# Optimization experiments

Measured on AMD Instinct MI355X. Metric: run time of the kernel, lower is better.

The kernel has to match this reference:

```python
import jax, jax.numpy as jnp
import numpy as np


def setup_inputs() -> dict:
    key = jax.random.key(0)
    k1, k2, k3, k4 = jax.random.split(key, 4)
    B, T, C, H = 8, 2048, 1024, 1024
    return {
        "x": jax.random.normal(k1, (B, T, C), dtype=jnp.float32),
        "Wk": jax.random.normal(k2, (H, C), dtype=jnp.float32),
        "Wq": jax.random.normal(k3, (H, C), dtype=jnp.float32),
        "Wv": jax.random.normal(k4, (H, C), dtype=jnp.float32),
    }


def reference(x, Wk, Wq, Wv):
    # x: [B, T, C]; Wk/Wq/Wv: [H, C] (torch Linear stores [fan_out, fan_in])
    B, T, C = x.shape
    k = jnp.einsum('btc,hc->bth', x, Wk)  # [B, T, H]
    q = jnp.einsum('btc,hc->bth', x, Wq)
    v = jnp.einsum('btc,hc->bth', x, Wv)
    # NOTE: source scales by n_embd (C) ** -0.5, not head_size
    wei = jnp.einsum('bth,bsh->bts', q, k) * (C ** -0.5)  # [B, T, T]
    causal = jnp.tril(jnp.ones((T, T), dtype=bool))
    wei = jnp.where(causal, wei, -jnp.inf)
    wei = jax.nn.softmax(wei, axis=-1)
    # Dropout omitted (inference behavior; p=0.5 train-only in source)
    out = jnp.einsum('bts,bsh->bth', wei, v)  # [B, T, H]
    return (out, wei)
```

## Files before the change

### kernel.cpp

```cpp
#include <hip/hip_runtime.h>
#include <hip/hip_bf16.h>


#define BB 8
#define TT 2048
#define CC 1024
#define HH 1024
#define BT (BB * TT)

typedef _Float16 f16x8 __attribute__((ext_vector_type(8)));
typedef _Float16 f16x4 __attribute__((ext_vector_type(4)));
typedef float f32x4 __attribute__((ext_vector_type(4)));

#define AS1 __attribute__((address_space(1)))
#define AS3 __attribute__((address_space(3)))

__device__ __forceinline__ void gld16(const _Float16* g, _Float16* lds) {
    __builtin_amdgcn_global_load_lds((AS1 const unsigned int*)g,
                                     (AS3 unsigned int*)lds, 16, 0, 0);
}

__global__ __launch_bounds__(256) void split_kernel(
    const float* __restrict__ src, _Float16* __restrict__ dh,
    _Float16* __restrict__ dl, int n)
{
    int i = (blockIdx.x * 256 + threadIdx.x) * 4;
    if (i >= n) return;
    float4 v = *(const float4*)(src + i);
    f16x4 h, l;
    h[0] = (_Float16)v.x; l[0] = (_Float16)(v.x - (float)h[0]);
    h[1] = (_Float16)v.y; l[1] = (_Float16)(v.y - (float)h[1]);
    h[2] = (_Float16)v.z; l[2] = (_Float16)(v.z - (float)h[2]);
    h[3] = (_Float16)v.w; l[3] = (_Float16)(v.w - (float)h[3]);
    *(f16x4*)&dh[i] = h;
    *(f16x4*)&dl[i] = l;
}

__global__ __launch_bounds__(256) void splitT_kernel(
    const float* __restrict__ W, _Float16* __restrict__ th,
    _Float16* __restrict__ tl)
{
    __shared__ float L[64][65];
    const int h0 = blockIdx.x * 64;
    const int c0 = blockIdx.y * 64;
    const int tid = threadIdx.x;
    {
        const int hl = tid >> 2;
        const int cs = (tid & 3) * 16;
#pragma unroll
        for (int jj = 0; jj < 16; jj += 4) {
            float4 v = *(const float4*)&W[(size_t)(h0 + hl) * CC + c0 + cs + jj];
            L[cs + jj + 0][hl] = v.x;
            L[cs + jj + 1][hl] = v.y;
            L[cs + jj + 2][hl] = v.z;
            L[cs + jj + 3][hl] = v.w;
        }
    }
    __syncthreads();
    const int c  = tid >> 2;
    const int hs = (tid & 3) * 16;
    f16x8 hv0, hv1, lv0, lv1;
#pragma unroll
    for (int i = 0; i < 8; ++i) {
        float a = L[c][hs + i], b = L[c][hs + 8 + i];
        hv0[i] = (_Float16)a; lv0[i] = (_Float16)(a - (float)hv0[i]);
        hv1[i] = (_Float16)b; lv1[i] = (_Float16)(b - (float)hv1[i]);
    }
    size_t o = (size_t)(c0 + c) * HH + h0 + hs;
    *(f16x8*)&th[o] = hv0; *(f16x8*)&th[o + 8] = hv1;
    *(f16x8*)&tl[o] = lv0; *(f16x8*)&tl[o + 8] = lv1;
}

__global__ __launch_bounds__(256, 2) void mm_kernel(
    const _Float16* __restrict__ aH, const _Float16* __restrict__ aL,
    const _Float16* __restrict__ bH, const _Float16* __restrict__ bL,
    _Float16* __restrict__ mtH, _Float16* __restrict__ mtL)
{
    __shared__ _Float16 Ah[4096], Al[4096], Bh[4096], Bl[4096];

    const int n0 = blockIdx.x * 128;
    const int m0 = blockIdx.y * 128;

    const int tid  = threadIdx.x;
    const int r0   = tid & 127;
    const int k0   = tid >> 7;
    const int wave = tid >> 6;
    const int lane = tid & 63;
    const int quad = lane >> 4;
    const int lrow = lane & 15;
    const int wr   = (wave >> 1) * 64;
    const int wc   = (wave & 1) * 64;

    const size_t ga = (size_t)(m0 + r0) * HH + k0 * 8;
    const size_t gb = (size_t)(n0 + r0) * HH + k0 * 8;
    const int lds0 = tid * 8, lds1 = (tid + 256) * 8;

    f32x4 acc[4][4] = {};

    for (int kc = 0; kc < HH; kc += 32) {
        __syncthreads();
        gld16(aH + ga + kc,      &Ah[lds0]);
        gld16(aH + ga + kc + 16, &Ah[lds1]);
        gld16(aL + ga + kc,      &Al[lds0]);
        gld16(aL + ga + kc + 16, &Al[lds1]);
        gld16(bH + gb + kc,      &Bh[lds0]);
        gld16(bH + gb + kc + 16, &Bh[lds1]);
        gld16(bL + gb + kc,      &Bl[lds0]);
        gld16(bL + gb + kc + 16, &Bl[lds1]);
        __syncthreads();

        f16x8 ahf[4], alf[4], bhf[4], blf[4];
#pragma unroll
        for (int i = 0; i < 4; ++i) {
            ahf[i] = *(const f16x8*)&Ah[(quad * 128 + wr + i * 16 + lrow) * 8];
            alf[i] = *(const f16x8*)&Al[(quad * 128 + wr + i * 16 + lrow) * 8];
            bhf[i] = *(const f16x8*)&Bh[(quad * 128 + wc + i * 16 + lrow) * 8];
            blf[i] = *(const f16x8*)&Bl[(quad * 128 + wc + i * 16 + lrow) * 8];
        }
#pragma unroll
        for (int i = 0; i < 4; ++i)
#pragma unroll
            for (int j = 0; j < 4; ++j) {
                acc[i][j] = __builtin_amdgcn_mfma_f32_16x16x32_f16(ahf[i], bhf[j], acc[i][j], 0, 0, 0);
                acc[i][j] = __builtin_amdgcn_mfma_f32_16x16x32_f16(ahf[i], blf[j], acc[i][j], 0, 0, 0);
                acc[i][j] = __builtin_amdgcn_mfma_f32_16x16x32_f16(alf[i], bhf[j], acc[i][j], 0, 0, 0);
            }
    }

#pragma unroll
    for (int i = 0; i < 4; ++i)
#pragma unroll
        for (int j = 0; j < 4; ++j) {
            int mm = m0 + wr + i * 16 + quad * 4;
            int nn = n0 + wc + j * 16 + lrow;
            f16x4 ph, pl;
#pragma unroll
            for (int r = 0; r < 4; ++r) {
                float val = acc[i][j][r];
                _Float16 h = (_Float16)val;
                ph[r] = h;
                pl[r] = (_Float16)(val - (float)h);
            }
            *(f16x4*)&mtH[(size_t)nn * CC + mm] = ph;
            *(f16x4*)&mtL[(size_t)nn * CC + mm] = pl;
        }
}

#define EPI_STRIDE 136
__global__ __launch_bounds__(256, 2) void pv_kernel(
    const _Float16* __restrict__ xh, const _Float16* __restrict__ xl,
    const _Float16* __restrict__ mtH, const _Float16* __restrict__ mtL,
    const _Float16* __restrict__ Wvh,
    _Float16* __restrict__ Ph, _Float16* __restrict__ Pl,
    _Float16* __restrict__ vT)
{
    __shared__ _Float16 S[49152];

    const int idx   = blockIdx.x;
    const int z     = idx >> 10;
    const int r     = idx & 1023;
    const int xcd   = r & 7;
    const int j7    = r >> 3;
    const int mtile = xcd * 16 + (j7 >> 3);
    const int ntile = j7 & 7;
    const int m0 = mtile * 128;
    const int n0 = ntile * 128;

    const int tid  = threadIdx.x;
    const int r0   = tid & 127;
    const int k0   = tid >> 7;
    const int wave = tid >> 6;
    const int lane = tid & 63;
    const int quad = lane >> 4;
    const int lrow = lane & 15;
    const int wr   = (wave >> 1) * 64;
    const int wc   = (wave & 1) * 64;

    const size_t ga = (size_t)(m0 + r0) * CC + k0 * 8;
    const size_t gb = (size_t)(n0 + r0) * CC + k0 * 8;
    const int lds0 = tid * 8, lds1 = (tid + 256) * 8;

    f32x4 acc[4][4] = {};

    if (z == 0) {
#define PV_STAGE0(kc_, sp_) do { \
        _Float16* Sb = S + (sp_) * 16384; \
        gld16(xh  + ga + (kc_),      &Sb[lds0]); \
        gld16(xh  + ga + (kc_) + 16, &Sb[lds1]); \
        gld16(xl  + ga + (kc_),      &Sb[4096 + lds0]); \
        gld16(xl  + ga + (kc_) + 16, &Sb[4096 + lds1]); \
        gld16(mtH + gb + (kc_),      &Sb[8192 + lds0]); \
        gld16(mtH + gb + (kc_) + 16, &Sb[8192 + lds1]); \
        gld16(mtL + gb + (kc_),      &Sb[12288 + lds0]); \
        gld16(mtL + gb + (kc_) + 16, &Sb[12288 + lds1]); \
    } while (0)
        PV_STAGE0(0, 0);
        PV_STAGE0(32, 1);
        int sl = 0;
        for (int kc = 0; kc < CC; kc += 32) {
            asm volatile("s_waitcnt vmcnt(8)" ::: "memory");
            __builtin_amdgcn_s_barrier();
            __builtin_amdgcn_sched_barrier(0);

            int kpre = kc + 64;
            if (kpre > CC - 32) kpre = CC - 32;
            int s2 = sl + 2; if (s2 >= 3) s2 -= 3;
            PV_STAGE0(kpre, s2);

            const _Float16* Ah = S + sl * 16384;
            const _Float16* Al = Ah + 4096;
            const _Float16* Bh = Ah + 8192;
            const _Float16* Bl = Ah + 12288;

            f16x8 ahf[4], alf[4], bhf[4], blf[4];
#pragma unroll
            for (int i = 0; i < 4; ++i) {
                ahf[i] = *(const f16x8*)&Ah[(quad * 128 + wr + i * 16 + lrow) * 8];
                alf[i] = *(const f16x8*)&Al[(quad * 128 + wr + i * 16 + lrow) * 8];
                bhf[i] = *(const f16x8*)&Bh[(quad * 128 + wc + i * 16 + lrow) * 8];
                blf[i] = *(const f16x8*)&Bl[(quad * 128 + wc + i * 16 + lrow) * 8];
            }
            __builtin_amdgcn_s_setprio(1);
#pragma unroll
            for (int i = 0; i < 4; ++i)
#pragma unroll
                for (int j = 0; j < 4; ++j) {
                    acc[i][j] = __builtin_amdgcn_mfma_f32_16x16x32_f16(ahf[i], bhf[j], acc[i][j], 0, 0, 0);
                    acc[i][j] = __builtin_amdgcn_mfma_f32_16x16x32_f16(ahf[i], blf[j], acc[i][j], 0, 0, 0);
                    acc[i][j] = __builtin_amdgcn_mfma_f32_16x16x32_f16(alf[i], bhf[j], acc[i][j], 0, 0, 0);
                }
            __builtin_amdgcn_s_setprio(0);

            ++sl; if (sl == 3) sl = 0;
        }
    } else {
#define PV_STAGE1(kc_, sp_) do { \
        _Float16* Sb = S + (sp_) * 8192; \
        gld16(xh  + ga + (kc_),      &Sb[lds0]); \
        gld16(xh  + ga + (kc_) + 16, &Sb[lds1]); \
        gld16(Wvh + gb + (kc_),      &Sb[4096 + lds0]); \
        gld16(Wvh + gb + (kc_) + 16, &Sb[4096 + lds1]); \
    } while (0)
        PV_STAGE1(0, 0);
        PV_STAGE1(32, 1);
        int sl = 0;
        for (int kc = 0; kc < CC; kc += 32) {
            asm volatile("s_waitcnt vmcnt(4)" ::: "memory");
            __builtin_amdgcn_s_barrier();
            __builtin_amdgcn_sched_barrier(0);

            int kpre = kc + 64;
            if (kpre > CC - 32) kpre = CC - 32;
            int s2 = sl + 2; if (s2 >= 3) s2 -= 3;
            PV_STAGE1(kpre, s2);

            const _Float16* Ah = S + sl * 8192;
            const _Float16* Bh = Ah + 4096;

            f16x8 ahf[4], bhf[4];
#pragma unroll
            for (int i = 0; i < 4; ++i) {
                ahf[i] = *(const f16x8*)&Ah[(quad * 128 + wr + i * 16 + lrow) * 8];
                bhf[i] = *(const f16x8*)&Bh[(quad * 128 + wc + i * 16 + lrow) * 8];
            }
            __builtin_amdgcn_s_setprio(1);
#pragma unroll
            for (int i = 0; i < 4; ++i)
#pragma unroll
                for (int j = 0; j < 4; ++j)
                    acc[i][j] = __builtin_amdgcn_mfma_f32_16x16x32_f16(ahf[i], bhf[j], acc[i][j], 0, 0, 0);
            __builtin_amdgcn_s_setprio(0);

            ++sl; if (sl == 3) sl = 0;
        }
    }

    asm volatile("s_waitcnt vmcnt(0)" ::: "memory");
    __syncthreads();

    if (z == 1) {
#pragma unroll
        for (int i = 0; i < 4; ++i)
#pragma unroll
            for (int j = 0; j < 4; ++j) {
                int hl = wc + j * 16 + lrow;
                int tl = wr + i * 16 + quad * 4;
                f16x4 p;
#pragma unroll
                for (int rr = 0; rr < 4; ++rr) p[rr] = (_Float16)acc[i][j][rr];
                *(f16x4*)&S[hl * EPI_STRIDE + tl] = p;
            }
        __syncthreads();
        const int bi  = mtile >> 4;
        const int t0g = (mtile & 15) * 128;
        _Float16* vb = vT + (size_t)bi * HH * TT;
#pragma unroll
        for (int rr = 0; rr < 128; rr += 16) {
            int h = rr + (tid >> 4);
            int t = (tid & 15) * 8;
            f16x8 val = *(const f16x8*)&S[h * EPI_STRIDE + t];
            *(f16x8*)&vb[(size_t)(n0 + h) * TT + t0g + t] = val;
        }
    } else {
#pragma unroll
        for (int i = 0; i < 4; ++i)
#pragma unroll
            for (int j = 0; j < 4; ++j) {
                int tl = wr + i * 16 + quad * 4;
                int cl = wc + j * 16 + lrow;
#pragma unroll
                for (int rr = 0; rr < 4; ++rr)
                    S[(tl + rr) * EPI_STRIDE + cl] = (_Float16)acc[i][j][rr];
            }
        __syncthreads();
#pragma unroll
        for (int rr = 0; rr < 128; rr += 16) {
            int t = rr + (tid >> 4);
            int c = (tid & 15) * 8;
            f16x8 val = *(const f16x8*)&S[t * EPI_STRIDE + c];
            *(f16x8*)&Ph[(size_t)(m0 + t) * CC + n0 + c] = val;
        }
        __syncthreads();
#pragma unroll
        for (int i = 0; i < 4; ++i)
#pragma unroll
            for (int j = 0; j < 4; ++j) {
                int tl = wr + i * 16 + quad * 4;
                int cl = wc + j * 16 + lrow;
#pragma unroll
                for (int rr = 0; rr < 4; ++rr) {
                    float val = acc[i][j][rr];
                    _Float16 h = (_Float16)val;
                    S[(tl + rr) * EPI_STRIDE + cl] = (_Float16)(val - (float)h);
                }
            }
        __syncthreads();
#pragma unroll
        for (int rr = 0; rr < 128; rr += 16) {
            int t = rr + (tid >> 4);
            int c = (tid & 15) * 8;
            f16x8 val = *(const f16x8*)&S[t * EPI_STRIDE + c];
            *(f16x8*)&Pl[(size_t)(m0 + t) * CC + n0 + c] = val;
        }
    }
}

__global__ __launch_bounds__(256, 2) void logits_kernel(
    const _Float16* __restrict__ Ph, const _Float16* __restrict__ Pl,
    const _Float16* __restrict__ xh, const _Float16* __restrict__ xl,
    float* __restrict__ wei)
{
    __shared__ _Float16 S[49152];

    const int id  = blockIdx.x;
    const int b   = id & 7;
    const int tri = id >> 3;
    int tt = (int)((sqrtf(8.0f * (float)tri + 1.0f) - 1.0f) * 0.5f);
    while ((tt + 1) * (tt + 2) / 2 <= tri) ++tt;
    while (tt * (tt + 1) / 2 > tri) --tt;
    const int st = tri - tt * (tt + 1) / 2;

    const size_t base = (size_t)b * TT * CC;
    float* wb = wei + (size_t)b * TT * TT;
    const int m0 = tt * 128;
    const int n0 = st * 128;

    const int tid  = threadIdx.x;
    const int r0   = tid & 127;
    const int k0   = tid >> 7;
    const int wave = tid >> 6;
    const int lane = tid & 63;
    const int quad = lane >> 4;
    const int lrow = lane & 15;
    const int wr   = (wave >> 1) * 64;
    const int wc   = (wave & 1) * 64;

    const size_t ga = base + (size_t)(m0 + r0) * CC + k0 * 8;
    const size_t gb = base + (size_t)(n0 + r0) * CC + k0 * 8;
    const int lds0 = tid * 8, lds1 = (tid + 256) * 8;

    f32x4 acc[4][4] = {};

#define LG_STAGE(kc_, sp_) do { \
    _Float16* Sb = S + (sp_) * 16384; \
    gld16(Ph + ga + (kc_),      &Sb[lds0]); \
    gld16(Ph + ga + (kc_) + 16, &Sb[lds1]); \
    gld16(Pl + ga + (kc_),      &Sb[4096 + lds0]); \
    gld16(Pl + ga + (kc_) + 16, &Sb[4096 + lds1]); \
    gld16(xh + gb + (kc_),      &Sb[8192 + lds0]); \
    gld16(xh + gb + (kc_) + 16, &Sb[8192 + lds1]); \
    gld16(xl + gb + (kc_),      &Sb[12288 + lds0]); \
    gld16(xl + gb + (kc_) + 16, &Sb[12288 + lds1]); \
} while (0)

    LG_STAGE(0, 0);
    LG_STAGE(32, 1);

    int sl = 0;
    for (int kc = 0; kc < CC; kc += 32) {
        asm volatile("s_waitcnt vmcnt(8)" ::: "memory");
        __builtin_amdgcn_s_barrier();
        __builtin_amdgcn_sched_barrier(0);

        int kpre = kc + 64;
        if (kpre > CC - 32) kpre = CC - 32;
        int s2 = sl + 2; if (s2 >= 3) s2 -= 3;
        LG_STAGE(kpre, s2);

        const _Float16* Ah = S + sl * 16384;
        const _Float16* Al = Ah + 4096;
        const _Float16* Bh = Ah + 8192;
        const _Float16* Bl = Ah + 12288;

        f16x8 ahf[4], alf[4], bhf[4], blf[4];
#pragma unroll
        for (int i = 0; i < 4; ++i) {
            ahf[i] = *(const f16x8*)&Ah[(quad * 128 + wr + i * 16 + lrow) * 8];
            alf[i] = *(const f16x8*)&Al[(quad * 128 + wr + i * 16 + lrow) * 8];
            bhf[i] = *(const f16x8*)&Bh[(quad * 128 + wc + i * 16 + lrow) * 8];
            blf[i] = *(const f16x8*)&Bl[(quad * 128 + wc + i * 16 + lrow) * 8];
        }
        __builtin_amdgcn_s_setprio(1);
#pragma unroll
        for (int i = 0; i < 4; ++i)
#pragma unroll
            for (int j = 0; j < 4; ++j) {
                acc[i][j] = __builtin_amdgcn_mfma_f32_16x16x32_f16(ahf[i], bhf[j], acc[i][j], 0, 0, 0);
                acc[i][j] = __builtin_amdgcn_mfma_f32_16x16x32_f16(ahf[i], blf[j], acc[i][j], 0, 0, 0);
                acc[i][j] = __builtin_amdgcn_mfma_f32_16x16x32_f16(alf[i], bhf[j], acc[i][j], 0, 0, 0);
            }
        __builtin_amdgcn_s_setprio(0);

        ++sl; if (sl == 3) sl = 0;
    }

    asm volatile("s_waitcnt vmcnt(0)" ::: "memory");

    const float scale = 0.03125f;
#pragma unroll
    for (int i = 0; i < 4; ++i)
#pragma unroll
        for (int j = 0; j < 4; ++j)
#pragma unroll
            for (int r = 0; r < 4; ++r) {
                int rr = wr + i * 16 + quad * 4 + r;
                int cc = wc + j * 16 + lrow;
                wb[(size_t)(m0 + rr) * TT + n0 + cc] = acc[i][j][r] * scale;
            }
}

__global__ __launch_bounds__(256) void softmax_kernel(
    float* __restrict__ wei, _Float16* __restrict__ wei16)
{
    const int t = blockIdx.x;
    const int b = blockIdx.y;
    float* row = wei + (size_t)b * TT * TT + (size_t)t * TT;
    _Float16* row16 = wei16 + (size_t)b * TT * TT + (size_t)t * TT;
    const int n = t + 1;
    const int tid = threadIdx.x;
    const int base = tid * 8;

    float vals[8];
    if (base < n) {
        float4 v0 = *(const float4*)&row[base];
        float4 v1 = *(const float4*)&row[base + 4];
        vals[0] = v0.x; vals[1] = v0.y; vals[2] = v0.z; vals[3] = v0.w;
        vals[4] = v1.x; vals[5] = v1.y; vals[6] = v1.z; vals[7] = v1.w;
    } else {
#pragma unroll
        for (int i = 0; i < 8; ++i) vals[i] = -INFINITY;
    }

    float mx = -INFINITY;
#pragma unroll
    for (int i = 0; i < 8; ++i) {
        if (base + i >= n) vals[i] = -INFINITY;
        mx = fmaxf(mx, vals[i]);
    }
#pragma unroll
    for (int off = 32; off > 0; off >>= 1)
        mx = fmaxf(mx, __shfl_down(mx, off));

    __shared__ float redm[4];
    __shared__ float reds[4];
    if ((tid & 63) == 0) redm[tid >> 6] = mx;
    __syncthreads();
    const float m = fmaxf(fmaxf(redm[0], redm[1]), fmaxf(redm[2], redm[3]));

    float sum = 0.f;
#pragma unroll
    for (int i = 0; i < 8; ++i) {
        vals[i] = __expf(vals[i] - m);
        sum += vals[i];
    }
#pragma unroll
    for (int off = 32; off > 0; off >>= 1)
        sum += __shfl_down(sum, off);
    if ((tid & 63) == 0) reds[tid >> 6] = sum;
    __syncthreads();
    const float inv = 1.0f / (reds[0] + reds[1] + reds[2] + reds[3]);

    f16x8 h;
#pragma unroll
    for (int i = 0; i < 8; ++i) {
        float w = vals[i] * inv;
        vals[i] = w;
        h[i] = (_Float16)w;
    }
    *(float4*)&row[base]     = make_float4(vals[0], vals[1], vals[2], vals[3]);
    *(float4*)&row[base + 4] = make_float4(vals[4], vals[5], vals[6], vals[7]);
    *(f16x8*)&row16[base]    = h;
}

__global__ __launch_bounds__(256, 3) void out_kernel(
    const _Float16* __restrict__ wei16, const _Float16* __restrict__ vT,
    float* __restrict__ out)
{
    __shared__ _Float16 S[24576];

    const int id = blockIdx.x;
    const int b  = id & 7;
    const int r  = id >> 3;
    const int tt = 15 - (r >> 3);
    const int nb = r & 7;

    const _Float16* wb = wei16 + (size_t)b * TT * TT;
    const _Float16* vb = vT    + (size_t)b * HH * TT;
    float*          ob = out   + (size_t)b * TT * HH;

    const int m0 = tt * 128;
    const int n0 = nb * 128;
    const int kend = (tt + 1) * 128;

    const int tid  = threadIdx.x;
    const int r0   = tid & 127;
    const int k0   = tid >> 7;
    const int wave = tid >> 6;
    const int lane = tid & 63;
    const int quad = lane >> 4;
    const int lrow = lane & 15;
    const int wr   = (wave >> 1) * 64;
    const int wc   = (wave & 1) * 64;

    const size_t ga = (size_t)(m0 + r0) * TT + k0 * 8;
    const size_t gb = (size_t)(n0 + r0) * TT + k0 * 8;
    const int lds0 = tid * 8, lds1 = (tid + 256) * 8;

    f32x4 acc[4][4] = {};

#define OUT_STAGE(kc_, sp_) do { \
    _Float16* Sb = S + (sp_) * 8192; \
    gld16(wb + ga + (kc_),      &Sb[lds0]); \
    gld16(wb + ga + (kc_) + 16, &Sb[lds1]); \
    gld16(vb + gb + (kc_),      &Sb[4096 + lds0]); \
    gld16(vb + gb + (kc_) + 16, &Sb[4096 + lds1]); \
} while (0)

    OUT_STAGE(0, 0);
    OUT_STAGE(32, 1);

    int sl = 0;
    for (int kc = 0; kc < kend; kc += 32) {
        asm volatile("s_waitcnt vmcnt(4)" ::: "memory");
        __builtin_amdgcn_s_barrier();
        __builtin_amdgcn_sched_barrier(0);

        int kpre = kc + 64;
        if (kpre > kend - 32) kpre = kend - 32;
        int s2 = sl + 2; if (s2 >= 3) s2 -= 3;
        OUT_STAGE(kpre, s2);

        const _Float16* Ah = S + sl * 8192;
        const _Float16* Bh = Ah + 4096;

        f16x8 ahf[4], bhf[4];
#pragma unroll
        for (int i = 0; i < 4; ++i) {
            ahf[i] = *(const f16x8*)&Ah[(quad * 128 + wr + i * 16 + lrow) * 8];
            bhf[i] = *(const f16x8*)&Bh[(quad * 128 + wc + i * 16 + lrow) * 8];
        }
        __builtin_amdgcn_s_setprio(1);
#pragma unroll
        for (int i = 0; i < 4; ++i)
#pragma unroll
            for (int j = 0; j < 4; ++j)
                acc[i][j] = __builtin_amdgcn_mfma_f32_16x16x32_f16(ahf[i], bhf[j], acc[i][j], 0, 0, 0);
        __builtin_amdgcn_s_setprio(0);

        ++sl; if (sl == 3) sl = 0;
    }

    asm volatile("s_waitcnt vmcnt(0)" ::: "memory");

#pragma unroll
    for (int i = 0; i < 4; ++i)
#pragma unroll
        for (int j = 0; j < 4; ++j)
#pragma unroll
            for (int r2 = 0; r2 < 4; ++r2) {
                int rr = wr + i * 16 + quad * 4 + r2;
                int cc = wc + j * 16 + lrow;
                ob[(size_t)(m0 + rr) * HH + n0 + cc] = acc[i][j][r2];
            }
}

extern "C" void kernel_launch(void* const* d_in, const int* in_sizes, int n_in,
                              void* d_out, int out_size, void* d_ws, size_t ws_size,
                              hipStream_t stream)
{
    const float* x  = (const float*)d_in[0];
    const float* Wk = (const float*)d_in[1];
    const float* Wq = (const float*)d_in[2];
    const float* Wv = (const float*)d_in[3];

    const size_t NX = (size_t)BT * CC;
    const size_t NW = (size_t)HH * CC;

    float* out = (float*)d_out;
    float* wei = out + (size_t)BT * HH;

    _Float16* WqTh = (_Float16*)out;
    _Float16* WqTl = WqTh + NW;
    _Float16* WkTh = WqTl + NW;
    _Float16* WkTl = WkTh + NW;
    _Float16* Wvh  = WkTl + NW;
    _Float16* Wvl  = Wvh  + NW;
    _Float16* MTh  = Wvl  + NW;
    _Float16* MTl  = MTh  + NW;

    _Float16* xh = (_Float16*)d_ws;
    _Float16* xl = xh + NX;
    _Float16* Ph = xl + NX;
    _Float16* Pl = Ph + NX;
    _Float16* vT = Pl + NX;
    _Float16* wei16 = (_Float16*)d_ws;

    split_kernel<<<dim3(NX / 1024), 256, 0, stream>>>(x, xh, xl, (int)NX);
    splitT_kernel<<<dim3(HH / 64, CC / 64), 256, 0, stream>>>(Wq, WqTh, WqTl);
    splitT_kernel<<<dim3(HH / 64, CC / 64), 256, 0, stream>>>(Wk, WkTh, WkTl);
    split_kernel<<<dim3(NW / 1024), 256, 0, stream>>>(Wv, Wvh, Wvl, (int)NW);

    mm_kernel<<<dim3(CC / 128, CC / 128), 256, 0, stream>>>(
        WqTh, WqTl, WkTh, WkTl, MTh, MTl);
    pv_kernel<<<dim3(2048), 256, 0, stream>>>(
        xh, xl, MTh, MTl, Wvh, Ph, Pl, vT);
    logits_kernel<<<dim3(136 * BB), 256, 0, stream>>>(
        Ph, Pl, xh, xl, wei);
    softmax_kernel<<<dim3(TT, BB), 256, 0, stream>>>(wei, wei16);
    out_kernel<<<dim3(128 * BB), 256, 0, stream>>>(wei16, vT, out);
}
```

Baseline: 832.5 us.

## Split projection kernel and use 128x256 tiles with 512 threads for logits

The fused pv_kernel, which picked between a P branch and a V branch by block index, becomes two kernels. The split-precision P projection (pv0) and the logits GEMM now use 128x256 block tiles with 8 waves and a larger three-stage LDS buffer, so each loaded A tile is reused across twice as many columns. The causal logits tile map is rebuilt for 256-wide column tiles, which computes some extra above-diagonal blocks that softmax masks anyway. The setprio hints around the MFMA loops are dropped. The larger LDS footprint and register use may limit occupancy.

```diff
diff --git a/kernel.cpp b/kernel.cpp
--- a/kernel.cpp
+++ b/kernel.cpp
@@ -146,21 +146,120 @@
         }
 }
 
-#define EPI_STRIDE 136
-__global__ __launch_bounds__(256, 2) void pv_kernel(
+__global__ __launch_bounds__(512, 2) void pv0_kernel(
     const _Float16* __restrict__ xh, const _Float16* __restrict__ xl,
     const _Float16* __restrict__ mtH, const _Float16* __restrict__ mtL,
-    const _Float16* __restrict__ Wvh,
-    _Float16* __restrict__ Ph, _Float16* __restrict__ Pl,
+    _Float16* __restrict__ Ph, _Float16* __restrict__ Pl)
+{
+    __shared__ _Float16 S[73728];
+
+    const int id  = blockIdx.x;
+    const int xcd = id & 7;
+    const int s   = id >> 3;
+    const int mtile = xcd * 16 + (s >> 2);
+    const int ntile = s & 3;
+    const int m0 = mtile * 128;
+    const int n0 = ntile * 256;
+
+    const int tid  = threadIdx.x;
+    const int wave = tid >> 6;
+    const int lane = tid & 63;
+    const int quad = lane >> 4;
+    const int lrow = lane & 15;
+    const int mw0  = (wave >> 2) * 64;
+    const int nw0  = (wave & 3) * 64;
+
+    const size_t gA = (size_t)(m0 + (tid & 127)) * CC + (tid >> 7) * 8;
+    const size_t gB = (size_t)(n0 + (tid & 255)) * CC + (tid >> 8) * 8;
+
+    f32x4 acc[4][4] = {};
+
+#define P0_STAGE(kc_, sp_) do { \
+    _Float16* Sb = S + (sp_) * 24576; \
+    gld16(xh  + gA + (kc_),      &Sb[tid * 8]); \
+    gld16(xl  + gA + (kc_),      &Sb[4096 + tid * 8]); \
+    gld16(mtH + gB + (kc_),      &Sb[8192 + tid * 8]); \
+    gld16(mtH + gB + (kc_) + 16, &Sb[8192 + (tid + 512) * 8]); \
+    gld16(mtL + gB + (kc_),      &Sb[16384 + tid * 8]); \
+    gld16(mtL + gB + (kc_) + 16, &Sb[16384 + (tid + 512) * 8]); \
+} while (0)
+
+    P0_STAGE(0, 0);
+    P0_STAGE(32, 1);
+    int sl = 0;
+    for (int kc = 0; kc < CC; kc += 32) {
+        asm volatile("s_waitcnt vmcnt(6)" ::: "memory");
+        __builtin_amdgcn_s_barrier();
+        __builtin_amdgcn_sched_barrier(0);
+
+        int ka = kc + 64; if (ka > CC - 32) ka = CC - 32;
+        int s2 = sl + 2; if (s2 >= 3) s2 -= 3;
+        P0_STAGE(ka, s2);
+
+        const _Float16* Ah = S + sl * 24576;
+        const _Float16* Al = Ah + 4096;
+        const _Float16* Bh = Ah + 8192;
+        const _Float16* Bl = Ah + 16384;
+
+        f16x8 ahf[4], alf[4], bhf[4], blf[4];
+#pragma unroll
+        for (int i = 0; i < 4; ++i) {
+            ahf[i] = *(const f16x8*)&Ah[(quad * 128 + mw0 + i * 16 + lrow) * 8];
+            alf[i] = *(const f16x8*)&Al[(quad * 128 + mw0 + i * 16 + lrow) * 8];
+            bhf[i] = *(const f16x8*)&Bh[(quad * 256 + nw0 + i * 16 + lrow) * 8];
+            blf[i] = *(const f16x8*)&Bl[(quad * 256 + nw0 + i * 16 + lrow) * 8];
+        }
+#pragma unroll
+        for (int i = 0; i < 4; ++i)
+#pragma unroll
+            for (int j = 0; j < 4; ++j) {
+                acc[i][j] = __builtin_amdgcn_mfma_f32_16x16x32_f16(ahf[i], bhf[j], acc[i][j], 0, 0, 0);
+                acc[i][j] = __builtin_amdgcn_mfma_f32_16x16x32_f16(ahf[i], blf[j], acc[i][j], 0, 0, 0);
+                acc[i][j] = __builtin_amdgcn_mfma_f32_16x16x32_f16(alf[i], bhf[j], acc[i][j], 0, 0, 0);
+            }
+
+        ++sl; if (sl == 3) sl = 0;
+    }
+
+    asm volatile("s_waitcnt vmcnt(0)" ::: "memory");
+
+#pragma unroll
+    for (int stream = 0; stream < 2; ++stream) {
+        _Float16* dst = stream ? Pl : Ph;
+        __syncthreads();
+#pragma unroll
+        for (int i = 0; i < 4; ++i)
+#pragma unroll
+            for (int j = 0; j < 4; ++j)
+#pragma unroll
+                for (int rr = 0; rr < 4; ++rr) {
+                    float v = acc[i][j][rr];
+                    _Float16 hi = (_Float16)v;
+                    S[(mw0 + i * 16 + quad * 4 + rr) * 264 + nw0 + j * 16 + lrow] =
+                        stream ? (_Float16)(v - (float)hi) : hi;
+                }
+        __syncthreads();
+#pragma unroll
+        for (int w = 0; w < 8; ++w) {
+            int x = w * 512 + tid;
+            int row = x >> 5;
+            int c8 = (x & 31) * 8;
+            *(f16x8*)&dst[(size_t)(m0 + row) * CC + n0 + c8] =
+                *(const f16x8*)&S[row * 264 + c8];
+        }
+    }
+}
+
+#define EPI_STRIDE 136
+__global__ __launch_bounds__(256, 3) void pv1_kernel(
+    const _Float16* __restrict__ xh, const _Float16* __restrict__ Wvh,
     _Float16* __restrict__ vT)
 {
-    __shared__ _Float16 S[49152];
-
-    const int idx   = blockIdx.x;
-    const int z     = idx >> 10;
-    const int r     = idx & 1023;
-    const int xcd   = r & 7;
-    const int j7    = r >> 3;
+    __shared__ _Float16 S[24576];
+
+    const int id  = blockIdx.x;
+    const int xcd = id & 7;
+    const int j7  = id >> 3;
     const int mtile = xcd * 16 + (j7 >> 3);
     const int ntile = j7 & 7;
     const int m0 = mtile * 128;
@@ -182,188 +281,248 @@
 
     f32x4 acc[4][4] = {};
 
-    if (z == 0) {
-#define PV_STAGE0(kc_, sp_) do { \
-        _Float16* Sb = S + (sp_) * 16384; \
-        gld16(xh  + ga + (kc_),      &Sb[lds0]); \
-        gld16(xh  + ga + (kc_) + 16, &Sb[lds1]); \
-        gld16(xl  + ga + (kc_),      &Sb[4096 + lds0]); \
-        gld16(xl  + ga + (kc_) + 16, &Sb[4096 + lds1]); \
-        gld16(mtH + gb + (kc_),      &Sb[8192 + lds0]); \
-        gld16(mtH + gb + (kc_) + 16, &Sb[8192 + lds1]); \
-        gld16(mtL + gb + (kc_),      &Sb[12288 + lds0]); \
-        gld16(mtL + gb + (kc_) + 16, &Sb[12288 + lds1]); \
-    } while (0)
-        PV_STAGE0(0, 0);
-        PV_STAGE0(32, 1);
-        int sl = 0;
-        for (int kc = 0; kc < CC; kc += 32) {
-            asm volatile("s_waitcnt vmcnt(8)" ::: "memory");
-            __builtin_amdgcn_s_barrier();
-            __builtin_amdgcn_sched_barrier(0);
-
-            int kpre = kc + 64;
-            if (kpre > CC - 32) kpre = CC - 32;
-            int s2 = sl + 2; if (s2 >= 3) s2 -= 3;
-            PV_STAGE0(kpre, s2);
-
-            const _Float16* Ah = S + sl * 16384;
-            const _Float16* Al = Ah + 4096;
-            const _Float16* Bh = Ah + 8192;
-            const _Float16* Bl = Ah + 12288;
-
-            f16x8 ahf[4], alf[4], bhf[4], blf[4];
-#pragma unroll
-            for (int i = 0; i < 4; ++i) {
-                ahf[i] = *(const f16x8*)&Ah[(quad * 128 + wr + i * 16 + lrow) * 8];
-                alf[i] = *(const f16x8*)&Al[(quad * 128 + wr + i * 16 + lrow) * 8];
-                bhf[i] = *(const f16x8*)&Bh[(quad * 128 + wc + i * 16 + lrow) * 8];
-                blf[i] = *(const f16x8*)&Bl[(quad * 128 + wc + i * 16 + lrow) * 8];
-            }
-            __builtin_amdgcn_s_setprio(1);
-#pragma unroll
-            for (int i = 0; i < 4; ++i)
-#pragma unroll
-                for (int j = 0; j < 4; ++j) {
-                    acc[i][j] = __builtin_amdgcn_mfma_f32_16x16x32_f16(ahf[i], bhf[j], acc[i][j], 0, 0, 0);
-                    acc[i][j] = __builtin_amdgcn_mfma_f32_16x16x32_f16(ahf[i], blf[j], acc[i][j], 0, 0, 0);
-                    acc[i][j] = __builtin_amdgcn_mfma_f32_16x16x32_f16(alf[i], bhf[j], acc[i][j], 0, 0, 0);
-                }
-            __builtin_amdgcn_s_setprio(0);
-
-            ++sl; if (sl == 3) sl = 0;
-        }
-    } else {
-#define PV_STAGE1(kc_, sp_) do { \
-        _Float16* Sb = S + (sp_) * 8192; \
-        gld16(xh  + ga + (kc_),      &Sb[lds0]); \
-        gld16(xh  + ga + (kc_) + 16, &Sb[lds1]); \
-        gld16(Wvh + gb + (kc_),      &Sb[4096 + lds0]); \
-        gld16(Wvh + gb + (kc_) + 16, &Sb[4096 + lds1]); \
-    } while (0)
-        PV_STAGE1(0, 0);
-        PV_STAGE1(32, 1);
-        int sl = 0;
-        for (int kc = 0; kc < CC; kc += 32) {
-            asm volatile("s_waitcnt vmcnt(4)" ::: "memory");
-            __builtin_amdgcn_s_barrier();
-            __builtin_amdgcn_sched_barrier(0);
-
-            int kpre = kc + 64;
-            if (kpre > CC - 32) kpre = CC - 32;
-            int s2 = sl + 2; if (s2 >= 3) s2 -= 3;
-            PV_STAGE1(kpre, s2);
-
-            const _Float16* Ah = S + sl * 8192;
-            const _Float16* Bh = Ah + 4096;
-
-            f16x8 ahf[4], bhf[4];
-#pragma unroll
-            for (int i = 0; i < 4; ++i) {
-                ahf[i] = *(const f16x8*)&Ah[(quad * 128 + wr + i * 16 + lrow) * 8];
-                bhf[i] = *(const f16x8*)&Bh[(quad * 128 + wc + i * 16 + lrow) * 8];
-            }
-            __builtin_amdgcn_s_setprio(1);
-#pragma unroll
-            for (int i = 0; i < 4; ++i)
-#pragma unroll
-                for (int j = 0; j < 4; ++j)
-                    acc[i][j] = __builtin_amdgcn_mfma_f32_16x16x32_f16(ahf[i], bhf[j], acc[i][j], 0, 0, 0);
-            __builtin_amdgcn_s_setprio(0);
-
-            ++sl; if (sl == 3) sl = 0;
-        }
+#define PV1_STAGE(kc_, sp_) do { \
+    _Float16* Sb = S + (sp_) * 8192; \
+    gld16(xh  + ga + (kc_),      &Sb[lds0]); \
+    gld16(xh  + ga + (kc_) + 16, &Sb[lds1]); \
+    gld16(Wvh + gb + (kc_),      &Sb[4096 + lds0]); \
+    gld16(Wvh + gb + (kc_) + 16, &Sb[4096 + lds1]); \
+} while (0)
+
+    PV1_STAGE(0, 0);
+    PV1_STAGE(32, 1);
+    int sl = 0;
+    for (int kc = 0; kc < CC; kc += 32) {
+        asm volatile("s_waitcnt vmcnt(4)" ::: "memory");
+        __builtin_amdgcn_s_barrier();
+        __builtin_amdgcn_sched_barrier(0);
+
+        int kpre = kc + 64;
+        if (kpre > CC - 32) kpre = CC - 32;
+        int s2 = sl + 2; if (s2 >= 3) s2 -= 3;
+        PV1_STAGE(kpre, s2);
+
+        const _Float16* Ah = S + sl * 8192;
+        const _Float16* Bh = Ah + 4096;
+
+        f16x8 ahf[4], bhf[4];
+#pragma unroll
+        for (int i = 0; i < 4; ++i) {
+            ahf[i] = *(const f16x8*)&Ah[(quad * 128 + wr + i * 16 + lrow) * 8];
+            bhf[i] = *(const f16x8*)&Bh[(quad * 128 + wc + i * 16 + lrow) * 8];
+        }
+#pragma unroll
+        for (int i = 0; i < 4; ++i)
+#pragma unroll
+            for (int j = 0; j < 4; ++j)
+                acc[i][j] = __builtin_amdgcn_mfma_f32_16x16x32_f16(ahf[i], bhf[j], acc[i][j], 0, 0, 0);
+
+        ++sl; if (sl == 3) sl = 0;
     }
 
     asm volatile("s_waitcnt vmcnt(0)" ::: "memory");
     __syncthreads();
 
-    if (z == 1) {
-#pragma unroll
-        for (int i = 0; i < 4; ++i)
-#pragma unroll
-            for (int j = 0; j < 4; ++j) {
-                int hl = wc + j * 16 + lrow;
-                int tl = wr + i * 16 + quad * 4;
-                f16x4 p;
-#pragma unroll
-                for (int rr = 0; rr < 4; ++rr) p[rr] = (_Float16)acc[i][j][rr];
-                *(f16x4*)&S[hl * EPI_STRIDE + tl] = p;
-            }
-        __syncthreads();
-        const int bi  = mtile >> 4;
-        const int t0g = (mtile & 15) * 128;
-        _Float16* vb = vT + (size_t)bi * HH * TT;
-#pragma unroll
-        for (int rr = 0; rr < 128; rr += 16) {
-            int h = rr + (tid >> 4);
-            int t = (tid & 15) * 8;
-            f16x8 val = *(const f16x8*)&S[h * EPI_STRIDE + t];
-            *(f16x8*)&vb[(size_t)(n0 + h) * TT + t0g + t] = val;
-        }
-    } else {
-#pragma unroll
-        for (int i = 0; i < 4; ++i)
-#pragma unroll
-            for (int j = 0; j < 4; ++j) {
-                int tl = wr + i * 16 + quad * 4;
-                int cl = wc + j * 16 + lrow;
-#pragma unroll
-                for (int rr = 0; rr < 4; ++rr)
-                    S[(tl + rr) * EPI_STRIDE + cl] = (_Float16)acc[i][j][rr];
-            }
-        __syncthreads();
-#pragma unroll
-        for (int rr = 0; rr < 128; rr += 16) {
-            int t = rr + (tid >> 4);
-            int c = (tid & 15) * 8;
-            f16x8 val = *(const f16x8*)&S[t * EPI_STRIDE + c];
-            *(f16x8*)&Ph[(size_t)(m0 + t) * CC + n0 + c] = val;
-        }
-        __syncthreads();
-#pragma unroll
-        for (int i = 0; i < 4; ++i)
-#pragma unroll
-            for (int j = 0; j < 4; ++j) {
-                int tl = wr + i * 16 + quad * 4;
-                int cl = wc + j * 16 + lrow;
-#pragma unroll
-                for (int rr = 0; rr < 4; ++rr) {
-                    float val = acc[i][j][rr];
-                    _Float16 h = (_Float16)val;
-                    S[(tl + rr) * EPI_STRIDE + cl] = (_Float16)(val - (float)h);
-                }
-            }
-        __syncthreads();
-#pragma unroll
-        for (int rr = 0; rr < 128; rr += 16) {
-            int t = rr + (tid >> 4);
-            int c = (tid & 15) * 8;
-            f16x8 val = *(const f16x8*)&S[t * EPI_STRIDE + c];
-            *(f16x8*)&Pl[(size_t)(m0 + t) * CC + n0 + c] = val;
-        }
-    }
-}
-
-__global__ __launch_bounds__(256, 2) void logits_kernel(
+#pragma unroll
+    for (int i = 0; i < 4; ++i)
+#pragma unroll
+        for (int j = 0; j < 4; ++j) {
+            int hl = wc + j * 16 + lrow;
+            int tl = wr + i * 16 + quad * 4;
+            f16x4 p;
+#pragma unroll
+            for (int rr = 0; rr < 4; ++rr) p[rr] = (_Float16)acc[i][j][rr];
+            *(f16x4*)&S[hl * EPI_STRIDE + tl] = p;
+        }
+    __syncthreads();
+    const int bi  = mtile >> 4;
+    const int t0g = (mtile & 15) * 128;
+    _Float16* vb = vT + (size_t)bi * HH * TT;
+#pragma unroll
+    for (int rr = 0; rr < 128; rr += 16) {
+        int h = rr + (tid >> 4);
+        int t = (tid & 15) * 8;
+        f16x8 val = *(const f16x8*)&S[h * EPI_STRIDE + t];
+        *(f16x8*)&vb[(size_t)(n0 + h) * TT + t0g + t] = val;
+    }
+}
+
+__global__ __launch_bounds__(512, 2) void logits_kernel(
     const _Float16* __restrict__ Ph, const _Float16* __restrict__ Pl,
     const _Float16* __restrict__ xh, const _Float16* __restrict__ xl,
     float* __restrict__ wei)
 {
-    __shared__ _Float16 S[49152];
-
-    const int id  = blockIdx.x;
-    const int b   = id & 7;
-    const int tri = id >> 3;
-    int tt = (int)((sqrtf(8.0f * (float)tri + 1.0f) - 1.0f) * 0.5f);
-    while ((tt + 1) * (tt + 2) / 2 <= tri) ++tt;
-    while (tt * (tt + 1) / 2 > tri) --tt;
-    const int st = tri - tt * (tt + 1) / 2;
+    __shared__ _Float16 S[73728];
+
+    const int id = blockIdx.x;
+    const int b  = id & 7;
+    const int q  = id >> 3;
+    int mt = 0, c0 = 0;
+    while (c0 + ((mt >> 1) + 1) <= q) { c0 += (mt >> 1) + 1; ++mt; }
+    const int nt = q - c0;
 
     const size_t base = (size_t)b * TT * CC;
     float* wb = wei + (size_t)b * TT * TT;
+    const int m0 = mt * 128;
+    const int n0 = nt * 256;
+
+    const int tid  = threadIdx.x;
+    const int wave = tid >> 6;
+    const int lane = tid & 63;
+    const int quad = lane >> 4;
+    const int lrow = lane & 15;
+    const int mw0  = (wave >> 2) * 64;
+    const int nw0  = (wave & 3) * 64;
+
+    const size_t gA = base + (size_t)(m0 + (tid & 127)) * CC + (tid >> 7) * 8;
+    const size_t gB = base + (size_t)(n0 + (tid & 255)) * CC + (tid >> 8) * 8;
+
+    f32x4 acc[4][4] = {};
+
+#define LG_STAGE(kc_, sp_) do { \
+    _Float16* Sb = S + (sp_) * 24576; \
+    gld16(Ph + gA + (kc_),      &Sb[tid * 8]); \
+    gld16(Pl + gA + (kc_),      &Sb[4096 + tid * 8]); \
+    gld16(xh + gB + (kc_),      &Sb[8192 + tid * 8]); \
+    gld16(xh + gB + (kc_) + 16, &Sb[8192 + (tid + 512) * 8]); \
+    gld16(xl + gB + (kc_),      &Sb[16384 + tid * 8]); \
+    gld16(xl + gB + (kc_) + 16, &Sb[16384 + (tid + 512) * 8]); \
+} while (0)
+
+    LG_STAGE(0, 0);
+    LG_STAGE(32, 1);
+    int sl = 0;
+    for (int kc = 0; kc < CC; kc += 32) {
+        asm volatile("s_waitcnt vmcnt(6)" ::: "memory");
+        __builtin_amdgcn_s_barrier();
+        __builtin_amdgcn_sched_barrier(0);
+
+        int ka = kc + 64; if (ka > CC - 32) ka = CC - 32;
+        int s2 = sl + 2; if (s2 >= 3) s2 -= 3;
+        LG_STAGE(ka, s2);
+
+        const _Float16* Ah = S + sl * 24576;
+        const _Float16* Al = Ah + 4096;
+        const _Float16* Bh = Ah + 8192;
+        const _Float16* Bl = Ah + 16384;
+
+        f16x8 ahf[4], alf[4], bhf[4], blf[4];
+#pragma unroll
+        for (int i = 0; i < 4; ++i) {
+            ahf[i] = *(const f16x8*)&Ah[(quad * 128 + mw0 + i * 16 + lrow) * 8];
+            alf[i] = *(const f16x8*)&Al[(quad * 128 + mw0 + i * 16 + lrow) * 8];
+            bhf[i] = *(const f16x8*)&Bh[(quad * 256 + nw0 + i * 16 + lrow) * 8];
+            blf[i] = *(const f16x8*)&Bl[(quad * 256 + nw0 + i * 16 + lrow) * 8];
+        }
+#pragma unroll
+        for (int i = 0; i < 4; ++i)
+#pragma unroll
+            for (int j = 0; j < 4; ++j) {
+                acc[i][j] = __builtin_amdgcn_mfma_f32_16x16x32_f16(ahf[i], bhf[j], acc[i][j], 0, 0, 0);
+                acc[i][j] = __builtin_amdgcn_mfma_f32_16x16x32_f16(ahf[i], blf[j], acc[i][j], 0, 0, 0);
+                acc[i][j] = __builtin_amdgcn_mfma_f32_16x16x32_f16(alf[i], bhf[j], acc[i][j], 0, 0, 0);
+            }
+
+        ++sl; if (sl == 3) sl = 0;
+    }
+
+    asm volatile("s_waitcnt vmcnt(0)" ::: "memory");
+
+    const float scale = 0.03125f;
+#pragma unroll
+    for (int i = 0; i < 4; ++i)
+#pragma unroll
+        for (int j = 0; j < 4; ++j)
+#pragma unroll
+            for (int r = 0; r < 4; ++r) {
+                int rr = mw0 + i * 16 + quad * 4 + r;
+                int cc = nw0 + j * 16 + lrow;
+                wb[(size_t)(m0 + rr) * TT + n0 + cc] = acc[i][j][r] * scale;
+            }
+}
+
+__global__ __launch_bounds__(256) void softmax_kernel(
+    float* __restrict__ wei, _Float16* __restrict__ wei16)
+{
+    const int t = blockIdx.x;
+    const int b = blockIdx.y;
+    float* row = wei + (size_t)b * TT * TT + (size_t)t * TT;
+    _Float16* row16 = wei16 + (size_t)b * TT * TT + (size_t)t * TT;
+    const int n = t + 1;
+    const int tid = threadIdx.x;
+    const int base = tid * 8;
+
+    float vals[8];
+    if (base < n) {
+        float4 v0 = *(const float4*)&row[base];
+        float4 v1 = *(const float4*)&row[base + 4];
+        vals[0] = v0.x; vals[1] = v0.y; vals[2] = v0.z; vals[3] = v0.w;
+        vals[4] = v1.x; vals[5] = v1.y; vals[6] = v1.z; vals[7] = v1.w;
+    } else {
+#pragma unroll
+        for (int i = 0; i < 8; ++i) vals[i] = -INFINITY;
+    }
+
+    float mx = -INFINITY;
+#pragma unroll
+    for (int i = 0; i < 8; ++i) {
+        if (base + i >= n) vals[i] = -INFINITY;
+        mx = fmaxf(mx, vals[i]);
+    }
+#pragma unroll
+    for (int off = 32; off > 0; off >>= 1)
+        mx = fmaxf(mx, __shfl_down(mx, off));
+
+    __shared__ float redm[4];
+    __shared__ float reds[4];
+    if ((tid & 63) == 0) redm[tid >> 6] = mx;
+    __syncthreads();
+    const float m = fmaxf(fmaxf(redm[0], redm[1]), fmaxf(redm[2], redm[3]));
+
+    float sum = 0.f;
+#pragma unroll
+    for (int i = 0; i < 8; ++i) {
+        vals[i] = __expf(vals[i] - m);
+        sum += vals[i];
+    }
+#pragma unroll
+    for (int off = 32; off > 0; off >>= 1)
+        sum += __shfl_down(sum, off);
+    if ((tid & 63) == 0) reds[tid >> 6] = sum;
+    __syncthreads();
+    const float inv = 1.0f / (reds[0] + reds[1] + reds[2] + reds[3]);
+
+    f16x8 h;
+#pragma unroll
+    for (int i = 0; i < 8; ++i) {
+        float w = vals[i] * inv;
+        vals[i] = w;
+        h[i] = (_Float16)w;
+    }
+    *(float4*)&row[base]     = make_float4(vals[0], vals[1], vals[2], vals[3]);
+    *(float4*)&row[base + 4] = make_float4(vals[4], vals[5], vals[6], vals[7]);
+    *(f16x8*)&row16[base]    = h;
+}
+
+__global__ __launch_bounds__(256, 3) void out_kernel(
+    const _Float16* __restrict__ wei16, const _Float16* __restrict__ vT,
+    float* __restrict__ out)
+{
+    __shared__ _Float16 S[24576];
+
+    const int id = blockIdx.x;
+    const int b  = id & 7;
+    const int r  = id >> 3;
+    const int tt = 15 - (r >> 3);
+    const int nb = r & 7;
+
+    const _Float16* wb = wei16 + (size_t)b * TT * TT;
+    const _Float16* vb = vT    + (size_t)b * HH * TT;
+    float*          ob = out   + (size_t)b * TT * HH;
+
     const int m0 = tt * 128;
-    const int n0 = st * 128;
+    const int n0 = nb * 128;
+    const int kend = (tt + 1) * 128;
 
     const int tid  = threadIdx.x;
     const int r0   = tid & 127;
@@ -375,173 +534,6 @@
     const int wr   = (wave >> 1) * 64;
     const int wc   = (wave & 1) * 64;
 
-    const size_t ga = base + (size_t)(m0 + r0) * CC + k0 * 8;
-    const size_t gb = base + (size_t)(n0 + r0) * CC + k0 * 8;
-    const int lds0 = tid * 8, lds1 = (tid + 256) * 8;
-
-    f32x4 acc[4][4] = {};
-
-#define LG_STAGE(kc_, sp_) do { \
-    _Float16* Sb = S + (sp_) * 16384; \
-    gld16(Ph + ga + (kc_),      &Sb[lds0]); \
-    gld16(Ph + ga + (kc_) + 16, &Sb[lds1]); \
-    gld16(Pl + ga + (kc_),      &Sb[4096 + lds0]); \
-    gld16(Pl + ga + (kc_) + 16, &Sb[4096 + lds1]); \
-    gld16(xh + gb + (kc_),      &Sb[8192 + lds0]); \
-    gld16(xh + gb + (kc_) + 16, &Sb[8192 + lds1]); \
-    gld16(xl + gb + (kc_),      &Sb[12288 + lds0]); \
-    gld16(xl + gb + (kc_) + 16, &Sb[12288 + lds1]); \
-} while (0)
-
-    LG_STAGE(0, 0);
-    LG_STAGE(32, 1);
-
-    int sl = 0;
-    for (int kc = 0; kc < CC; kc += 32) {
-        asm volatile("s_waitcnt vmcnt(8)" ::: "memory");
-        __builtin_amdgcn_s_barrier();
-        __builtin_amdgcn_sched_barrier(0);
-
-        int kpre = kc + 64;
-        if (kpre > CC - 32) kpre = CC - 32;
-        int s2 = sl + 2; if (s2 >= 3) s2 -= 3;
-        LG_STAGE(kpre, s2);
-
-        const _Float16* Ah = S + sl * 16384;
-        const _Float16* Al = Ah + 4096;
-        const _Float16* Bh = Ah + 8192;
-        const _Float16* Bl = Ah + 12288;
-
-        f16x8 ahf[4], alf[4], bhf[4], blf[4];
-#pragma unroll
-        for (int i = 0; i < 4; ++i) {
-            ahf[i] = *(const f16x8*)&Ah[(quad * 128 + wr + i * 16 + lrow) * 8];
-            alf[i] = *(const f16x8*)&Al[(quad * 128 + wr + i * 16 + lrow) * 8];
-            bhf[i] = *(const f16x8*)&Bh[(quad * 128 + wc + i * 16 + lrow) * 8];
-            blf[i] = *(const f16x8*)&Bl[(quad * 128 + wc + i * 16 + lrow) * 8];
-        }
-        __builtin_amdgcn_s_setprio(1);
-#pragma unroll
-        for (int i = 0; i < 4; ++i)
-#pragma unroll
-            for (int j = 0; j < 4; ++j) {
-                acc[i][j] = __builtin_amdgcn_mfma_f32_16x16x32_f16(ahf[i], bhf[j], acc[i][j], 0, 0, 0);
-                acc[i][j] = __builtin_amdgcn_mfma_f32_16x16x32_f16(ahf[i], blf[j], acc[i][j], 0, 0, 0);
-                acc[i][j] = __builtin_amdgcn_mfma_f32_16x16x32_f16(alf[i], bhf[j], acc[i][j], 0, 0, 0);
-            }
-        __builtin_amdgcn_s_setprio(0);
-
-        ++sl; if (sl == 3) sl = 0;
-    }
-
-    asm volatile("s_waitcnt vmcnt(0)" ::: "memory");
-
-    const float scale = 0.03125f;
-#pragma unroll
-    for (int i = 0; i < 4; ++i)
-#pragma unroll
-        for (int j = 0; j < 4; ++j)
-#pragma unroll
-            for (int r = 0; r < 4; ++r) {
-                int rr = wr + i * 16 + quad * 4 + r;
-                int cc = wc + j * 16 + lrow;
-                wb[(size_t)(m0 + rr) * TT + n0 + cc] = acc[i][j][r] * scale;
-            }
-}
-
-__global__ __launch_bounds__(256) void softmax_kernel(
-    float* __restrict__ wei, _Float16* __restrict__ wei16)
-{
-    const int t = blockIdx.x;
-    const int b = blockIdx.y;
-    float* row = wei + (size_t)b * TT * TT + (size_t)t * TT;
-    _Float16* row16 = wei16 + (size_t)b * TT * TT + (size_t)t * TT;
-    const int n = t + 1;
-    const int tid = threadIdx.x;
-    const int base = tid * 8;
-
-    float vals[8];
-    if (base < n) {
-        float4 v0 = *(const float4*)&row[base];
-        float4 v1 = *(const float4*)&row[base + 4];
-        vals[0] = v0.x; vals[1] = v0.y; vals[2] = v0.z; vals[3] = v0.w;
-        vals[4] = v1.x; vals[5] = v1.y; vals[6] = v1.z; vals[7] = v1.w;
-    } else {
-#pragma unroll
-        for (int i = 0; i < 8; ++i) vals[i] = -INFINITY;
-    }
-
-    float mx = -INFINITY;
-#pragma unroll
-    for (int i = 0; i < 8; ++i) {
-        if (base + i >= n) vals[i] = -INFINITY;
-        mx = fmaxf(mx, vals[i]);
-    }
-#pragma unroll
-    for (int off = 32; off > 0; off >>= 1)
-        mx = fmaxf(mx, __shfl_down(mx, off));
-
-    __shared__ float redm[4];
-    __shared__ float reds[4];
-    if ((tid & 63) == 0) redm[tid >> 6] = mx;
-    __syncthreads();
-    const float m = fmaxf(fmaxf(redm[0], redm[1]), fmaxf(redm[2], redm[3]));
-
-    float sum = 0.f;
-#pragma unroll
-    for (int i = 0; i < 8; ++i) {
-        vals[i] = __expf(vals[i] - m);
-        sum += vals[i];
-    }
-#pragma unroll
-    for (int off = 32; off > 0; off >>= 1)
-        sum += __shfl_down(sum, off);
-    if ((tid & 63) == 0) reds[tid >> 6] = sum;
-    __syncthreads();
-    const float inv = 1.0f / (reds[0] + reds[1] + reds[2] + reds[3]);
-
-    f16x8 h;
-#pragma unroll
-    for (int i = 0; i < 8; ++i) {
-        float w = vals[i] * inv;
-        vals[i] = w;
-        h[i] = (_Float16)w;
-    }
-    *(float4*)&row[base]     = make_float4(vals[0], vals[1], vals[2], vals[3]);
-    *(float4*)&row[base + 4] = make_float4(vals[4], vals[5], vals[6], vals[7]);
-    *(f16x8*)&row16[base]    = h;
-}
-
-__global__ __launch_bounds__(256, 3) void out_kernel(
-    const _Float16* __restrict__ wei16, const _Float16* __restrict__ vT,
-    float* __restrict__ out)
-{
-    __shared__ _Float16 S[24576];
-
-    const int id = blockIdx.x;
-    const int b  = id & 7;
-    const int r  = id >> 3;
-    const int tt = 15 - (r >> 3);
-    const int nb = r & 7;
-
-    const _Float16* wb = wei16 + (size_t)b * TT * TT;
-    const _Float16* vb = vT    + (size_t)b * HH * TT;
-    float*          ob = out   + (size_t)b * TT * HH;
-
-    const int m0 = tt * 128;
-    const int n0 = nb * 128;
-    const int kend = (tt + 1) * 128;
-
-    const int tid  = threadIdx.x;
-    const int r0   = tid & 127;
-    const int k0   = tid >> 7;
-    const int wave = tid >> 6;
-    const int lane = tid & 63;
-    const int quad = lane >> 4;
-    const int lrow = lane & 15;
-    const int wr   = (wave >> 1) * 64;
-    const int wc   = (wave & 1) * 64;
-
     const size_t ga = (size_t)(m0 + r0) * TT + k0 * 8;
     const size_t gb = (size_t)(n0 + r0) * TT + k0 * 8;
     const int lds0 = tid * 8, lds1 = (tid + 256) * 8;
@@ -579,13 +571,11 @@
             ahf[i] = *(const f16x8*)&Ah[(quad * 128 + wr + i * 16 + lrow) * 8];
             bhf[i] = *(const f16x8*)&Bh[(quad * 128 + wc + i * 16 + lrow) * 8];
         }
-        __builtin_amdgcn_s_setprio(1);
 #pragma unroll
         for (int i = 0; i < 4; ++i)
 #pragma unroll
             for (int j = 0; j < 4; ++j)
                 acc[i][j] = __builtin_amdgcn_mfma_f32_16x16x32_f16(ahf[i], bhf[j], acc[i][j], 0, 0, 0);
-        __builtin_amdgcn_s_setprio(0);
 
         ++sl; if (sl == 3) sl = 0;
     }
@@ -642,9 +632,11 @@
 
     mm_kernel<<<dim3(CC / 128, CC / 128), 256, 0, stream>>>(
         WqTh, WqTl, WkTh, WkTl, MTh, MTl);
-    pv_kernel<<<dim3(2048), 256, 0, stream>>>(
-        xh, xl, MTh, MTl, Wvh, Ph, Pl, vT);
-    logits_kernel<<<dim3(136 * BB), 256, 0, stream>>>(
+    pv0_kernel<<<dim3(512), 512, 0, stream>>>(
+        xh, xl, MTh, MTl, Ph, Pl);
+    pv1_kernel<<<dim3(1024), 256, 0, stream>>>(
+        xh, Wvh, vT);
+    logits_kernel<<<dim3(72 * BB), 512, 0, stream>>>(
         Ph, Pl, xh, xl, wei);
     softmax_kernel<<<dim3(TT, BB), 256, 0, stream>>>(wei, wei16);
     out_kernel<<<dim3(128 * BB), 256, 0, stream>>>(wei16, vT, out);
```

Result: slower. 857.4 us (+3.0%).
